# Performance work log

Hardware: AMD Instinct MI355X
Metric: run time of the kernel (lower is better)

Reference implementation:

```python
import jax, jax.numpy as jnp
import numpy as np

FACTOR = 1  # init factor -> top_k = int(factor * log(L))


def setup_inputs() -> dict:
    key = jax.random.key(0)
    kq, kk, kv = jax.random.split(key, 3)
    B, L, H, E = 16, 2048, 8, 64
    shape = (B, L, H, E)
    return {
        "queries": jax.random.normal(kq, shape, dtype=jnp.float32),
        "keys": jax.random.normal(kk, shape, dtype=jnp.float32),
        "values": jax.random.normal(kv, shape, dtype=jnp.float32),
    }


def reference(queries, keys, values):
    B, L, H, E = queries.shape
    # seq lens equal -> torch's pad/truncate branch is a no-op slice
    q = jnp.transpose(queries, (0, 2, 3, 1))  # [B,H,E,L]
    k = jnp.transpose(keys, (0, 2, 3, 1))
    v = jnp.transpose(values, (0, 2, 3, 1))

    # FFT-based circular cross-correlation along time
    qf = jnp.fft.rfft(q, axis=-1)
    kf = jnp.fft.rfft(k, axis=-1)
    corr = jnp.fft.irfft(qf * jnp.conj(kf), n=L, axis=-1)  # [B,H,E,L]

    top_k = int(FACTOR * np.log(L))  # static: 7 for L=2048
    mean_value = corr.mean(axis=(1, 2))  # mean over head then variates -> [B,L]
    # global (batch-averaged) top-k delays, shared across batch (training path)
    _, topk_index = jax.lax.top_k(mean_value.mean(axis=0), top_k)  # [k]
    # per-batch weights at those delays, softmax over k
    w = jax.nn.softmax(mean_value[:, topk_index], axis=-1)  # [B,k]

    # torch.roll(v, -d, -1)[..., t] == v[..., (t + d) % L]
    idx = (jnp.arange(L)[None, :] + topk_index[:, None]) % L  # [k,L]
    gathered = v[..., idx]  # [B,H,E,k,L]
    agg = jnp.einsum('bhekl,bk->bhel', gathered, w)  # weighted delay aggregation

    return jnp.transpose(agg, (0, 3, 1, 2))  # back to [B,L,H,E]
```

## Files before the change

### kernel.cpp

```cpp
#include <hip/hip_runtime.h>
#include <hip/hip_bf16.h>
#include <hip/hip_fp16.h>
#include <math.h>


#define B_ 16
#define L_ 2048
#define H_ 8
#define E_ 64
#define NBLK 512
#define K_ 7
#define RS_ 2178

#define PART_OFF 0ull
#define MV_OFF   8388608ull
#define TK_OFF   (MV_OFF + 131072ull)
#define W_OFF    (TK_OFF + 64ull)

__device__ __forceinline__ float2 cadd(float2 a, float2 b) { return make_float2(a.x + b.x, a.y + b.y); }
__device__ __forceinline__ float2 csub(float2 a, float2 b) { return make_float2(a.x - b.x, a.y - b.y); }
__device__ __forceinline__ float2 cmul(float2 a, float2 b) {
  return make_float2(fmaf(a.x, b.x, -a.y * b.y), fmaf(a.x, b.y, a.y * b.x));
}
__device__ __forceinline__ float2 cis(float ang) { float s, c; sincosf(ang, &s, &c); return make_float2(c, s); }

template<int S> __device__ __forceinline__ float2 rot90(float2 z) {
  return (S < 0) ? make_float2(z.y, -z.x) : make_float2(-z.y, z.x);
}
template<int S> __device__ __forceinline__ void dft4(float2& a, float2& b, float2& c, float2& d) {
  float2 t0 = cadd(a, c), t1 = csub(a, c), t2 = cadd(b, d), t3 = rot90<S>(csub(b, d));
  a = cadd(t0, t2); c = csub(t0, t2); b = cadd(t1, t3); d = csub(t1, t3);
}
template<int S> __device__ __forceinline__ void dft8(float2 v[8]) {
  const float RT = 0.70710678118654752f;
  const float SR = (S < 0) ? -RT : RT;
  float2 a0 = cadd(v[0], v[4]), a1 = cadd(v[1], v[5]), a2 = cadd(v[2], v[6]), a3 = cadd(v[3], v[7]);
  float2 b0 = csub(v[0], v[4]), b1 = csub(v[1], v[5]), b2 = csub(v[2], v[6]), b3 = csub(v[3], v[7]);
  b1 = cmul(b1, make_float2(RT, SR));
  b2 = rot90<S>(b2);
  b3 = cmul(b3, make_float2(-RT, SR));
  dft4<S>(a0, a1, a2, a3);
  dft4<S>(b0, b1, b2, b3);
  v[0] = a0; v[2] = a1; v[4] = a2; v[6] = a3;
  v[1] = b0; v[3] = b1; v[5] = b2; v[7] = b3;
}
__device__ __forceinline__ int sg(int e) { return e + (e >> 4); }

__device__ __forceinline__ float2 ld16(const __half2* p) { return __half22float2(*p); }
__device__ __forceinline__ void st16(__half2* p, float2 v) { *p = __float22half2_rn(v); }

__global__ __launch_bounds__(512) void fft_corr_kernel(
    const float* __restrict__ q, const float* __restrict__ k,
    float2* __restrict__ part) {
  extern __shared__ __half2 dbuf[];
  int tid = threadIdx.x;
  int t = tid & 255;
  int half = tid >> 8;
  int j2 = t & 31, j3 = t & 3;
  int l = blockIdx.x;
  int eg = l & 3, h = (l >> 2) & 7, b = l >> 5;
  size_t base = (size_t)b * (L_ * H_ * E_) + (size_t)h * E_ + eg * 16;

  {
    int f4 = tid & 3, tau0 = tid >> 2;
#pragma unroll 4
    for (int m = 0; m < 16; ++m) {
      int tau = tau0 + 128 * m;
      size_t a = base + (size_t)tau * (H_ * E_) + f4 * 4;
      float4 q4 = *(const float4*)(q + a);
      float4 k4 = *(const float4*)(k + a);
      int sp = sg(tau);
      st16(&dbuf[(4 * f4 + 0) * RS_ + sp], make_float2(q4.x, k4.x));
      st16(&dbuf[(4 * f4 + 1) * RS_ + sp], make_float2(q4.y, k4.y));
      st16(&dbuf[(4 * f4 + 2) * RS_ + sp], make_float2(q4.z, k4.z));
      st16(&dbuf[(4 * f4 + 3) * RS_ + sp], make_float2(q4.w, k4.w));
    }
  }
  __syncthreads();

  float2 tw1[7], tw2[7], tw3[7];
  {
    float2 w1 = cis(-6.283185307179586f * (float)t  / 2048.0f);
    float2 w2 = cis(-6.283185307179586f * (float)j2 / 256.0f);
    float2 w3 = cis(-6.283185307179586f * (float)j3 / 32.0f);
    tw1[0] = w1; tw2[0] = w2; tw3[0] = w3;
#pragma unroll
    for (int kk = 1; kk < 7; ++kk) {
      tw1[kk] = cmul(tw1[kk - 1], w1);
      tw2[kk] = cmul(tw2[kk - 1], w2);
      tw3[kk] = cmul(tw3[kk - 1], w3);
    }
  }
  int base2 = (t >> 5) * 256 + j2;
  int base3 = (t >> 2) * 32 + j3;
  float2 acc[8];
#pragma unroll
  for (int kk = 0; kk < 8; ++kk) acc[kk] = make_float2(0.f, 0.f);

  for (int p = 0; p < 4; ++p) {
    __half2* A  = dbuf + (size_t)(4 * p + 2 * half) * RS_;
    __half2* Bf = A + RS_;
    float2 va[8], vb[8];
#pragma unroll
    for (int m = 0; m < 8; ++m) { va[m] = ld16(&A[sg(t + 256 * m)]); vb[m] = ld16(&Bf[sg(t + 256 * m)]); }
    dft8<-1>(va); dft8<-1>(vb);
#pragma unroll
    for (int kk = 1; kk < 8; ++kk) { va[kk] = cmul(va[kk], tw1[kk - 1]); vb[kk] = cmul(vb[kk], tw1[kk - 1]); }
#pragma unroll
    for (int kk = 0; kk < 8; ++kk) { st16(&A[sg(t + 256 * kk)], va[kk]); st16(&Bf[sg(t + 256 * kk)], vb[kk]); }
    __syncthreads();
#pragma unroll
    for (int m = 0; m < 8; ++m) { va[m] = ld16(&A[sg(base2 + 32 * m)]); vb[m] = ld16(&Bf[sg(base2 + 32 * m)]); }
    dft8<-1>(va); dft8<-1>(vb);
#pragma unroll
    for (int kk = 1; kk < 8; ++kk) { va[kk] = cmul(va[kk], tw2[kk - 1]); vb[kk] = cmul(vb[kk], tw2[kk - 1]); }
#pragma unroll
    for (int kk = 0; kk < 8; ++kk) { st16(&A[sg(base2 + 32 * kk)], va[kk]); st16(&Bf[sg(base2 + 32 * kk)], vb[kk]); }
    __syncthreads();
#pragma unroll
    for (int m = 0; m < 8; ++m) { va[m] = ld16(&A[sg(base3 + 4 * m)]); vb[m] = ld16(&Bf[sg(base3 + 4 * m)]); }
    dft8<-1>(va); dft8<-1>(vb);
#pragma unroll
    for (int kk = 1; kk < 8; ++kk) { va[kk] = cmul(va[kk], tw3[kk - 1]); vb[kk] = cmul(vb[kk], tw3[kk - 1]); }
#pragma unroll
    for (int kk = 0; kk < 8; ++kk) { st16(&A[sg(base3 + 4 * kk)], va[kk]); st16(&Bf[sg(base3 + 4 * kk)], vb[kk]); }
    __syncthreads();
#pragma unroll
    for (int kk = 0; kk < 8; ++kk) { va[kk] = ld16(&A[sg(8 * t + kk)]); vb[kk] = ld16(&Bf[sg(8 * t + kk)]); }
    dft4<-1>(va[0], va[1], va[2], va[3]); dft4<-1>(va[4], va[5], va[6], va[7]);
    dft4<-1>(vb[0], vb[1], vb[2], vb[3]); dft4<-1>(vb[4], vb[5], vb[6], vb[7]);
#pragma unroll
    for (int kk = 0; kk < 8; ++kk) { st16(&A[sg(8 * t + kk)], va[kk]); st16(&Bf[sg(8 * t + kk)], vb[kk]); }
    __syncthreads();
#pragma unroll
    for (int kk = 0; kk < 8; ++kk) {
      int pos = 8 * t + kk;
      int f  = ((pos >> 8) & 7) | (((pos >> 5) & 7) << 3) | (((pos >> 2) & 7) << 6) | ((pos & 3) << 9);
      int fp = (2048 - f) & 2047;
      int pp = ((fp & 7) << 8) | (((fp >> 3) & 7) << 5) | (((fp >> 6) & 7) << 2) | ((fp >> 9) & 3);
      float2 Ax = va[kk], Bc = ld16(&A[sg(pp)]);
      acc[kk].x += 0.5f  * (Bc.x * Ax.y + Bc.y * Ax.x);
      acc[kk].y += 0.25f * (Ax.x * Ax.x + Ax.y * Ax.y - Bc.x * Bc.x - Bc.y * Bc.y);
      Ax = vb[kk]; Bc = ld16(&Bf[sg(pp)]);
      acc[kk].x += 0.5f  * (Bc.x * Ax.y + Bc.y * Ax.x);
      acc[kk].y += 0.25f * (Ax.x * Ax.x + Ax.y * Ax.y - Bc.x * Bc.x - Bc.y * Bc.y);
    }
  }
  {
    float* fre = (float*)dbuf + (size_t)(2 * half) * RS_;
    float* fim = fre + RS_;
#pragma unroll
    for (int kk = 0; kk < 8; ++kk) {
      int sp = sg(8 * t + kk);
      fre[sp] = acc[kk].x;
      fim[sp] = acc[kk].y;
    }
  }
  __syncthreads();
  {
    const float* r0 = (const float*)dbuf;
    const float* i0 = r0 + RS_;
    const float* r1 = r0 + 2 * RS_;
    const float* i1 = r0 + 3 * RS_;
    float2* prow = part + (size_t)l * L_;
#pragma unroll
    for (int m = 0; m < 4; ++m) {
      int p = tid + 512 * m;
      int sp = sg(p);
      prow[p] = make_float2(r0[sp] + r1[sp], i0[sp] + i1[sp]);
    }
  }
}

__global__ __launch_bounds__(256) void ifft_kernel(
    const float2* __restrict__ part, float* __restrict__ mv) {
  __shared__ float2 buf[2176];
  int t = threadIdx.x, b = blockIdx.x;
  int j2 = t & 31, j3 = t & 3;
  float2 tw1[7], tw2[7], tw3[7];
  {
    float2 w1 = cis(6.283185307179586f * (float)t  / 2048.0f);
    float2 w2 = cis(6.283185307179586f * (float)j2 / 256.0f);
    float2 w3 = cis(6.283185307179586f * (float)j3 / 32.0f);
    tw1[0] = w1; tw2[0] = w2; tw3[0] = w3;
#pragma unroll
    for (int kk = 1; kk < 7; ++kk) {
      tw1[kk] = cmul(tw1[kk - 1], w1);
      tw2[kk] = cmul(tw2[kk - 1], w2);
      tw3[kk] = cmul(tw3[kk - 1], w3);
    }
  }
  int base2 = (t >> 5) * 256 + j2;
  int base3 = (t >> 2) * 32 + j3;
  float2 u[8];
#pragma unroll
  for (int kk = 0; kk < 8; ++kk) u[kk] = make_float2(0.f, 0.f);
#pragma unroll 4
  for (int g = 0; g < 32; ++g) {
    const float4* rp = (const float4*)(part + (size_t)(b * 32 + g) * L_);
#pragma unroll
    for (int m = 0; m < 4; ++m) {
      float4 f = rp[4 * t + m];
      u[2 * m].x     += f.x; u[2 * m].y     += f.y;
      u[2 * m + 1].x += f.z; u[2 * m + 1].y += f.w;
    }
  }
  dft4<1>(u[0], u[1], u[2], u[3]);
  dft4<1>(u[4], u[5], u[6], u[7]);
#pragma unroll
  for (int kk = 0; kk < 8; ++kk) buf[sg(8 * t + kk)] = u[kk];
  __syncthreads();
  float2 v[8];
#pragma unroll
  for (int kk = 0; kk < 8; ++kk) v[kk] = buf[sg(base3 + 4 * kk)];
#pragma unroll
  for (int kk = 1; kk < 8; ++kk) v[kk] = cmul(v[kk], tw3[kk - 1]);
  dft8<1>(v);
  __syncthreads();
#pragma unroll
  for (int m = 0; m < 8; ++m) buf[sg(base3 + 4 * m)] = v[m];
  __syncthreads();
#pragma unroll
  for (int kk = 0; kk < 8; ++kk) v[kk] = buf[sg(base2 + 32 * kk)];
#pragma unroll
  for (int kk = 1; kk < 8; ++kk) v[kk] = cmul(v[kk], tw2[kk - 1]);
  dft8<1>(v);
  __syncthreads();
#pragma unroll
  for (int m = 0; m < 8; ++m) buf[sg(base2 + 32 * m)] = v[m];
  __syncthreads();
#pragma unroll
  for (int kk = 0; kk < 8; ++kk) v[kk] = buf[sg(t + 256 * kk)];
#pragma unroll
  for (int kk = 1; kk < 8; ++kk) v[kk] = cmul(v[kk], tw1[kk - 1]);
  dft8<1>(v);
  const float scale = 1.0f / (2048.0f * 512.0f);
#pragma unroll
  for (int m = 0; m < 8; ++m) mv[b * L_ + t + 256 * m] = v[m].x * scale;
}

__global__ __launch_bounds__(256) void topk_kernel(
    const float* __restrict__ mv, int* __restrict__ topk, float* __restrict__ wts) {
  __shared__ float av[2048];
  __shared__ float rv[256];
  __shared__ int   ri[256];
  __shared__ int   sidx[K_];
  int tid = threadIdx.x;
  for (int d = tid; d < 2048; d += 256) {
    float s = 0.f;
#pragma unroll
    for (int b = 0; b < B_; ++b) s += mv[b * L_ + d];
    av[d] = s;
  }
  __syncthreads();
  for (int kk = 0; kk < K_; ++kk) {
    float bv = -INFINITY; int bi = 0;
    for (int d = tid; d < 2048; d += 256) {
      float vv = av[d];
      if (vv > bv) { bv = vv; bi = d; }
    }
    rv[tid] = bv; ri[tid] = bi;
    __syncthreads();
    for (int off = 128; off > 0; off >>= 1) {
      if (tid < off) {
        float v2 = rv[tid + off]; int i2 = ri[tid + off];
        if (v2 > rv[tid] || (v2 == rv[tid] && i2 < ri[tid])) { rv[tid] = v2; ri[tid] = i2; }
      }
      __syncthreads();
    }
    if (tid == 0) { sidx[kk] = ri[0]; av[ri[0]] = -INFINITY; }
    __syncthreads();
  }
  if (tid < K_) topk[tid] = sidx[tid];
  if (tid < B_) {
    float xk[K_], m = -INFINITY;
#pragma unroll
    for (int kk = 0; kk < K_; ++kk) { xk[kk] = mv[tid * L_ + sidx[kk]]; m = fmaxf(m, xk[kk]); }
    float s = 0.f;
#pragma unroll
    for (int kk = 0; kk < K_; ++kk) { xk[kk] = expf(xk[kk] - m); s += xk[kk]; }
#pragma unroll
    for (int kk = 0; kk < K_; ++kk) wts[tid * K_ + kk] = xk[kk] / s;
  }
}

__global__ __launch_bounds__(256) void aggregate_kernel(
    const float4* __restrict__ v4, const int* __restrict__ topk,
    const float* __restrict__ wts, float4* __restrict__ out4) {
  __shared__ int   sidx[K_];
  __shared__ float sw[B_][K_];
  int tid = threadIdx.x;
  if (tid < K_) sidx[tid] = topk[tid];
  if (tid < B_ * K_) sw[tid / K_][tid % K_] = wts[tid];
  __syncthreads();
  int idx = blockIdx.x * 256 + tid;
  int c4  = idx & 127;
  int row = idx >> 7;
  int t   = row & (L_ - 1);
  int b   = row >> 11;
  float4 acc = make_float4(0.f, 0.f, 0.f, 0.f);
#pragma unroll
  for (int kk = 0; kk < K_; ++kk) {
    int s = t + sidx[kk];
    if (s >= L_) s -= L_;
    float w = sw[b][kk];
    float4 val = v4[((size_t)(b * L_ + s) << 7) + c4];
    acc.x += w * val.x; acc.y += w * val.y;
    acc.z += w * val.z; acc.w += w * val.w;
  }
  out4[idx] = acc;
}

extern "C" void kernel_launch(void* const* d_in, const int* in_sizes, int n_in,
                              void* d_out, int out_size, void* d_ws, size_t ws_size,
                              hipStream_t stream) {
  const float* q = (const float*)d_in[0];
  const float* k = (const float*)d_in[1];
  const float* v = (const float*)d_in[2];
  float* out = (float*)d_out;

  char* ws = (char*)d_ws;
  float2* part = (float2*)(ws + PART_OFF);
  float*  mv   = (float*) (ws + MV_OFF);
  int*    topk = (int*)   (ws + TK_OFF);
  float*  wts  = (float*) (ws + W_OFF);

  fft_corr_kernel<<<NBLK, 512, 16 * RS_ * 4, stream>>>(q, k, part);
  ifft_kernel<<<B_, 256, 0, stream>>>(part, mv);
  topk_kernel<<<1, 256, 0, stream>>>(mv, topk, wts);
  aggregate_kernel<<<(B_ * L_ * H_ * E_ / 4) / 256, 256, 0, stream>>>(
      (const float4*)v, topk, wts, (float4*)out);
}
```

Baseline: 159.6 us.

## Add pack kernel to transpose q/k into fp16 channel-major slabs, halve FFT block work

A new pack kernel converts q and k to interleaved half2 pairs and transposes them through shared memory into per-channel time-contiguous slabs in workspace. The FFT kernel then reads these slabs with contiguous loads instead of strided float4 gathers over the [B,L,H,E] layout. It also handles 8 channels per block instead of 16, doubling the block count and halving shared memory per block to raise occupancy. The cost is an extra global round trip of 64 MB of packed data, an extra launch, and twice as many partial rows to reduce in the inverse FFT kernel.

```diff
diff --git a/kernel.cpp b/kernel.cpp
--- a/kernel.cpp
+++ b/kernel.cpp
@@ -8,12 +8,12 @@
 #define L_ 2048
 #define H_ 8
 #define E_ 64
-#define NBLK 512
 #define K_ 7
 #define RS_ 2178
 
-#define PART_OFF 0ull
-#define MV_OFF   8388608ull
+#define Z_OFF    0ull
+#define PART_OFF 67108864ull
+#define MV_OFF   (PART_OFF + 16777216ull)
 #define TK_OFF   (MV_OFF + 131072ull)
 #define W_OFF    (TK_OFF + 64ull)
 
@@ -49,32 +49,63 @@
 __device__ __forceinline__ float2 ld16(const __half2* p) { return __half22float2(*p); }
 __device__ __forceinline__ void st16(__half2* p, float2 v) { *p = __float22half2_rn(v); }
 
+__global__ __launch_bounds__(512) void pack_kernel(
+    const float* __restrict__ q, const float* __restrict__ k,
+    float4* __restrict__ z) {
+  extern __shared__ float4 tile[];
+  int tid = threadIdx.x;
+  int l = blockIdx.x;
+  int tl = l & 63, b = l >> 6;
+  size_t rowbase = ((size_t)b * L_ + tl * 32) * 512;
+  const float4* q4 = (const float4*)(q + rowbase);
+  const float4* k4 = (const float4*)(k + rowbase);
+#pragma unroll
+  for (int pass = 0; pass < 8; ++pass) {
+    int m = pass * 512 + tid;
+    int j = m >> 7, cq = m & 127;
+    float4 qv = q4[j * 128 + cq];
+    float4 kv = k4[j * 128 + cq];
+    float4 pk;
+    ((__half2*)&pk)[0] = __float22half2_rn(make_float2(qv.x, kv.x));
+    ((__half2*)&pk)[1] = __float22half2_rn(make_float2(qv.y, kv.y));
+    ((__half2*)&pk)[2] = __float22half2_rn(make_float2(qv.z, kv.z));
+    ((__half2*)&pk)[3] = __float22half2_rn(make_float2(qv.w, kv.w));
+    tile[cq * 33 + j] = pk;
+  }
+  __syncthreads();
+  float4* slab = z + (size_t)l * 4096;
+#pragma unroll
+  for (int pass = 0; pass < 8; ++pass) {
+    int m = pass * 512 + tid;
+    int cq = m >> 5, j = m & 31;
+    slab[cq * 32 + j] = tile[cq * 33 + j];
+  }
+}
+
 __global__ __launch_bounds__(512) void fft_corr_kernel(
-    const float* __restrict__ q, const float* __restrict__ k,
-    float2* __restrict__ part) {
+    const float4* __restrict__ z, float2* __restrict__ part) {
   extern __shared__ __half2 dbuf[];
   int tid = threadIdx.x;
   int t = tid & 255;
   int half = tid >> 8;
   int j2 = t & 31, j3 = t & 3;
   int l = blockIdx.x;
-  int eg = l & 3, h = (l >> 2) & 7, b = l >> 5;
-  size_t base = (size_t)b * (L_ * H_ * E_) + (size_t)h * E_ + eg * 16;
-
-  {
-    int f4 = tid & 3, tau0 = tid >> 2;
-#pragma unroll 4
-    for (int m = 0; m < 16; ++m) {
-      int tau = tau0 + 128 * m;
-      size_t a = base + (size_t)tau * (H_ * E_) + f4 * 4;
-      float4 q4 = *(const float4*)(q + a);
-      float4 k4 = *(const float4*)(k + a);
-      int sp = sg(tau);
-      st16(&dbuf[(4 * f4 + 0) * RS_ + sp], make_float2(q4.x, k4.x));
-      st16(&dbuf[(4 * f4 + 1) * RS_ + sp], make_float2(q4.y, k4.y));
-      st16(&dbuf[(4 * f4 + 2) * RS_ + sp], make_float2(q4.z, k4.z));
-      st16(&dbuf[(4 * f4 + 3) * RS_ + sp], make_float2(q4.w, k4.w));
-    }
+  int cg = l & 63, b = l >> 6;
+  int cq0 = cg * 2;
+  const float4* zb = z + (size_t)b * 64 * 4096;
+
+#pragma unroll
+  for (int it = 0; it < 8; ++it) {
+    int m = it * 512 + tid;
+    int tl = m >> 6, inner = m & 63;
+    int cqr = inner >> 5, j = inner & 31;
+    float4 pk = zb[(size_t)tl * 4096 + (cq0 + cqr) * 32 + j];
+    int sp = sg(tl * 32 + j);
+    const __half2* hp = (const __half2*)&pk;
+    dbuf[(cqr * 4 + 0) * RS_ + sp] = hp[0];
+    dbuf[(cqr * 4 + 1) * RS_ + sp] = hp[1];
+    dbuf[(cqr * 4 + 2) * RS_ + sp] = hp[2];
+    dbuf[(cqr * 4 + 3) * RS_ + sp] = hp[3];
   }
   __syncthreads();
 
@@ -97,7 +128,7 @@
 #pragma unroll
   for (int kk = 0; kk < 8; ++kk) acc[kk] = make_float2(0.f, 0.f);
 
-  for (int p = 0; p < 4; ++p) {
+  for (int p = 0; p < 2; ++p) {
     __half2* A  = dbuf + (size_t)(4 * p + 2 * half) * RS_;
     __half2* Bf = A + RS_;
     float2 va[8], vb[8];
@@ -196,8 +227,8 @@
 #pragma unroll
   for (int kk = 0; kk < 8; ++kk) u[kk] = make_float2(0.f, 0.f);
 #pragma unroll 4
-  for (int g = 0; g < 32; ++g) {
-    const float4* rp = (const float4*)(part + (size_t)(b * 32 + g) * L_);
+  for (int g = 0; g < 64; ++g) {
+    const float4* rp = (const float4*)(part + (size_t)(b * 64 + g) * L_);
 #pragma unroll
     for (int m = 0; m < 4; ++m) {
       float4 f = rp[4 * t + m];
@@ -320,12 +351,14 @@
   float* out = (float*)d_out;
 
   char* ws = (char*)d_ws;
+  float4* z    = (float4*)(ws + Z_OFF);
   float2* part = (float2*)(ws + PART_OFF);
   float*  mv   = (float*) (ws + MV_OFF);
   int*    topk = (int*)   (ws + TK_OFF);
   float*  wts  = (float*) (ws + W_OFF);
 
-  fft_corr_kernel<<<NBLK, 512, 16 * RS_ * 4, stream>>>(q, k, part);
+  pack_kernel<<<B_ * 64, 512, 4224 * sizeof(float4), stream>>>(q, k, z);
+  fft_corr_kernel<<<B_ * 64, 512, 8 * RS_ * 4, stream>>>(z, part);
   ifft_kernel<<<B_, 256, 0, stream>>>(part, mv);
   topk_kernel<<<1, 256, 0, stream>>>(mv, topk, wts);
   aggregate_kernel<<<(B_ * L_ * H_ * E_ / 4) / 256, 256, 0, stream>>>(
```

Result: slower. 183.0 us (+14.7%).
